# Performance work log

Measured on AMD Instinct MI355X. Metric: run time of the kernel, lower is better.

## Reference

```python
import jax, jax.numpy as jnp
import numpy as np

SPIXELS = 1000
CLASSES = 21


def setup_inputs() -> dict:
    key = jax.random.key(0)
    k1, k2, k3, k4 = jax.random.split(key, 4)
    B, H, W = 8, 512, 512
    pred = jax.random.normal(k1, (B, CLASSES, H, W), dtype=jnp.float32)
    Laplace_W_c = jax.random.normal(k2, (B, SPIXELS, SPIXELS), dtype=jnp.float32)
    Laplace_L_c = jax.random.normal(k3, (B, SPIXELS, SPIXELS), dtype=jnp.float32)
    image_spiex = jax.random.randint(k4, (B, H, W), 0, SPIXELS, dtype=jnp.int32)
    return {"pred": pred, "Laplace_W_c": Laplace_W_c, "Laplace_L_c": Laplace_L_c, "image_spiex": image_spiex}


def reference(pred, Laplace_W_c, Laplace_L_c, image_spiex):
    B, _, H, W = pred.shape
    P = H * W
    # Faithful to original: permute(0,2,3,1) then reshape to [B, class_num, H*W]
    pred_r = jnp.transpose(pred, (0, 2, 3, 1)).reshape(B, CLASSES, P)  # [B, C, P]
    seg = image_spiex.reshape(B, P)  # [B, P] superpixel ids
    # result[b, c, s] = sum_{p: seg[b,p]==s} pred_r[b, c, p]  -- the bmm(pred, one_hot_mask)
    # expressed as an efficient segment-sum instead of materializing [B, P, SPIXELS].
    seg_sum = jax.vmap(
        lambda x, ids: jax.ops.segment_sum(x, ids, num_segments=SPIXELS)
    )(jnp.transpose(pred_r, (0, 2, 1)), seg)  # [B, S, C]
    result = jnp.transpose(seg_sum, (0, 2, 1))  # [B, C, S]
    # mask.sum() = count of (b, p, s) with seg[b,p] == s, i.e. pixels with valid ids
    mask_sum = jnp.sum(((seg >= 0) & (seg < SPIXELS)).astype(pred.dtype))
    result = result / (mask_sum + 1e-16)
    # trace(R @ L @ R^T) per batch, fused
    traces = jnp.einsum('bcs,bst,bct->b', result, Laplace_L_c, result)  # [B]
    loss = (2.0 / jnp.linalg.norm(Laplace_W_c)) * traces
    return jnp.mean(loss)
```

## Files before the change

### kernel.cpp

```cpp
#include <hip/hip_runtime.h>
#include <hip/hip_bf16.h>

#define SPIX 1000
#define NCLS 21
#define PP (512*512)
#define NB_IMG 8
#define EPB (NCLS*PP)

#define FWIN 32768
#define BLKS_PER_B (EPB / FWIN)
#define DUMP 1000

#define R_OFF   0
#define TR_OFF  (NB_IMG*NCLS*SPIX)
#define NS_OFF  (TR_OFF + NB_IMG)
#define CNT_OFF (NS_OFF + 1)
#define CTR_OFF (CNT_OFF + 1)
#define WS_FLOATS (CTR_OFF + 1)

__device__ __forceinline__ void fatomic_add(float* p, float v) {
    unsafeAtomicAdd(p, v);
}

__global__ __launch_bounds__(512, 8) void scatter_kernel(const float* __restrict__ pred,
                                                         const int* __restrict__ seg,
                                                         const float* __restrict__ W,
                                                         float* __restrict__ Rout,
                                                         float* __restrict__ ns,
                                                         float* __restrict__ cnt) {
    if (blockIdx.y == NB_IMG) {
        if (blockIdx.x < 128) {
            const float4* W4 = (const float4*)W;
            const int n4 = (NB_IMG * SPIX * SPIX) / 4;
            float s = 0.f;
            for (int i = blockIdx.x * 512 + threadIdx.x; i < n4; i += 128 * 512) {
                float4 v = W4[i];
                s += v.x*v.x + v.y*v.y + v.z*v.z + v.w*v.w;
            }
            #pragma unroll
            for (int off = 32; off; off >>= 1) s += __shfl_xor(s, off);
            if ((threadIdx.x & 63) == 0) fatomic_add(ns, s);
        } else {
            const int4* s4 = (const int4*)seg;
            const int n4 = (NB_IMG * PP) / 4;
            int c = 0;
            for (int i = (blockIdx.x - 128) * 512 + threadIdx.x; i < n4; i += 40 * 512) {
                int4 v = s4[i];
                c += ((unsigned)v.x < SPIX) + ((unsigned)v.y < SPIX) + ((unsigned)v.z < SPIX) + ((unsigned)v.w < SPIX);
            }
            float f = (float)c;
            #pragma unroll
            for (int off = 32; off; off >>= 1) f += __shfl_xor(f, off);
            if ((threadIdx.x & 63) == 0) fatomic_add(cnt, f);
        }
        return;
    }
    __shared__ float         Rw[8][1024];
    __shared__ unsigned char Mk[8][1024];
    const int b    = blockIdx.y;
    const int tid  = threadIdx.x;
    const int wave = tid >> 6;
    const unsigned char lane = (unsigned char)(tid & 63);
    const unsigned f0 = (unsigned)blockIdx.x * FWIN;
    const unsigned c0 = f0 >> 18;
    const unsigned p0 = f0 & (PP - 1);

    for (int i = tid; i < 8 * 1024; i += 512) ((float*)Rw)[i] = 0.f;
    __syncthreads();

    volatile float*         vR = Rw[wave];
    volatile unsigned char* vM = Mk[wave];
    float* aR = (float*)Rw[wave];

    const float* pb   = pred + (size_t)b * EPB;
    const int*   segb = seg + (size_t)b * PP + p0;

    for (int it = 0; it < FWIN / (512 * 4); ++it) {
        const int e0 = (it * 512 + tid) * 4;
        int4 sv = *(const int4*)(segb + e0);
        int sA[4]; float vA[4];
        {
            unsigned fk = f0 + (unsigned)e0;
            unsigned sp = fk / 21u;
            unsigned ch = fk - sp * 21u;
            #pragma unroll
            for (int k = 0; k < 4; ++k) {
                vA[k] = pb[(ch << 18) + sp];
                int s = (&sv.x)[k];
                sA[k] = ((unsigned)s < SPIX) ? s : DUMP;
                ch++;
                bool c21 = (ch == 21u);
                sp += c21 ? 1u : 0u;
                ch  = c21 ? 0u : ch;
            }
        }
        #pragma unroll
        for (int i = 0; i < 3; ++i)
            #pragma unroll
            for (int j = i + 1; j < 4; ++j) {
                bool e = (sA[j] == sA[i]) && (sA[i] != DUMP);
                vA[i] += e ? vA[j] : 0.f;
                sA[j]  = e ? DUMP  : sA[j];
            }
        #pragma unroll
        for (int k = 0; k < 4; ++k) vM[sA[k]] = lane;
        unsigned char rd[4];
        #pragma unroll
        for (int k = 0; k < 4; ++k) rd[k] = vM[sA[k]];
        float od[4];
        #pragma unroll
        for (int k = 0; k < 4; ++k) od[k] = vR[sA[k]];
        bool lose1[4];
        #pragma unroll
        for (int k = 0; k < 4; ++k) {
            lose1[k] = (rd[k] != lane);
            vR[lose1[k] ? DUMP : sA[k]] = od[k] + vA[k];
        }
        asm volatile("" ::: "memory");
        #pragma unroll
        for (int k = 0; k < 4; ++k) {
            if (lose1[k]) fatomic_add(&aR[sA[k]], vA[k]);
        }
    }
    __syncthreads();

    float* Rb = Rout + (size_t)b * NCLS * SPIX + (size_t)c0 * SPIX;
    for (int i = tid; i < SPIX; i += 512) {
        float a = 0.f;
        #pragma unroll
        for (int w = 0; w < 8; ++w) a += Rw[w][i];
        fatomic_add(&Rb[i], a);
    }
}

__global__ __launch_bounds__(512) void trace_kernel(const float* __restrict__ L,
                                                    const float* __restrict__ R,
                                                    float* __restrict__ traces,
                                                    const float* __restrict__ ns,
                                                    const float* __restrict__ cnt,
                                                    unsigned* __restrict__ ctr,
                                                    float* __restrict__ out) {
    __shared__ float Rl[NCLS * SPIX];
    const int b = blockIdx.y;
    const float* Rb = R + (size_t)b * NCLS * SPIX;
    for (int i = threadIdx.x; i < NCLS * SPIX; i += 512) Rl[i] = Rb[i];
    __syncthreads();

    const int wave = threadIdx.x >> 6;
    const int lane = threadIdx.x & 63;
    const float* Lb = L + (size_t)b * SPIX * SPIX;

    const int s0 = (blockIdx.x * 8 + wave) * 4;
    bool val[4];
    const float4* Lr[4];
    #pragma unroll
    for (int r = 0; r < 4; ++r) {
        int sr = s0 + r;
        val[r] = sr < SPIX;
        Lr[r] = (const float4*)(Lb + (size_t)(val[r] ? sr : (SPIX - 1)) * SPIX);
    }

    float acc[4][NCLS];
    #pragma unroll
    for (int r = 0; r < 4; ++r)
        #pragma unroll
        for (int c = 0; c < NCLS; ++c) acc[r][c] = 0.f;

    #pragma unroll
    for (int it = 0; it < 4; ++it) {
        int idx = it * 64 + lane;
        if (idx < SPIX / 4) {
            float4 l[4];
            #pragma unroll
            for (int r = 0; r < 4; ++r)
                l[r] = val[r] ? Lr[r][idx] : make_float4(0.f, 0.f, 0.f, 0.f);
            #pragma unroll
            for (int c = 0; c < NCLS; ++c) {
                float4 rr = *(const float4*)&Rl[c * SPIX + idx * 4];
                #pragma unroll
                for (int r = 0; r < 4; ++r)
                    acc[r][c] += l[r].x * rr.x + l[r].y * rr.y + l[r].z * rr.z + l[r].w * rr.w;
            }
        }
    }

    float partial = 0.f;
    #pragma unroll
    for (int c = 0; c < NCLS; ++c)
        #pragma unroll
        for (int r = 0; r < 4; ++r)
            if (val[r]) partial += Rl[c * SPIX + s0 + r] * acc[r][c];

    #pragma unroll
    for (int off = 32; off; off >>= 1) partial += __shfl_xor(partial, off);
    if (lane == 0) fatomic_add(&traces[b], partial);

    __syncthreads();
    if (threadIdx.x == 0) {
        __threadfence();
        unsigned old = atomicAdd(ctr, 1u);
        if (old == 32u * NB_IMG - 1u) {
            __threadfence();
            float t = 0.f;
            #pragma unroll
            for (int i = 0; i < NB_IMG; ++i)
                t += __hip_atomic_load(&traces[i], __ATOMIC_RELAXED, __HIP_MEMORY_SCOPE_AGENT);
            float denom = cnt[0] + 1e-16f;
            out[0] = (2.f / sqrtf(ns[0])) * t / (denom * denom) / (float)NB_IMG;
        }
    }
}

extern "C" void kernel_launch(void* const* d_in, const int* in_sizes, int n_in,
                              void* d_out, int out_size, void* d_ws, size_t ws_size,
                              hipStream_t stream) {
    const float* pred = (const float*)d_in[0];
    const float* Wc   = (const float*)d_in[1];
    const float* Lc   = (const float*)d_in[2];
    const int*   seg  = (const int*)d_in[3];
    float* ws = (float*)d_ws;
    float* out = (float*)d_out;

    hipMemsetAsync(d_ws, 0, WS_FLOATS * sizeof(float), stream);

    scatter_kernel<<<dim3(BLKS_PER_B, NB_IMG + 1), 512, 0, stream>>>(
        pred, seg, Wc, ws + R_OFF, ws + NS_OFF, ws + CNT_OFF);

    trace_kernel<<<dim3(32, NB_IMG), 512, 0, stream>>>(
        Lc, ws + R_OFF, ws + TR_OFF, ws + NS_OFF, ws + CNT_OFF,
        (unsigned*)(ws + CTR_OFF), out);
}
```

Baseline: 158.3 us.

## Reuse per-pixel conflict analysis across all classes and reduce partials deterministically

Each block now handles a window of 4096 pixels and loops over all 21 output channels. The superpixel-ID load, the within-thread duplicate detection and the two-round LDS conflict election run once per window instead of once per class window, and the resulting masks are reused for every class. Per-class block results go either to a partial buffer reduced by a new reduce_kernel, which avoids global atomics, or to atomics when the workspace is too small. The trade-offs are an extra kernel launch and partial-buffer traffic, lower occupancy (launch bounds drop to 4), and fewer blocks for the W-norm and count side tasks.

```diff
diff --git a/kernel.cpp b/kernel.cpp
--- a/kernel.cpp
+++ b/kernel.cpp
@@ -7,8 +7,9 @@
 #define NB_IMG 8
 #define EPB (NCLS*PP)
 
-#define FWIN 32768
-#define BLKS_PER_B (EPB / FWIN)
+#define WIN 4096
+#define WPB (PP/WIN)
+#define NBLK (WPB*NB_IMG)
 #define DUMP 1000
 
 #define R_OFF   0
@@ -17,23 +18,27 @@
 #define CNT_OFF (NS_OFF + 1)
 #define CTR_OFF (CNT_OFF + 1)
 #define WS_FLOATS (CTR_OFF + 1)
+#define RP_OFF  ((WS_FLOATS + 3) & ~3)
+#define RP_FLOATS ((size_t)NBLK * NCLS * SPIX)
 
 __device__ __forceinline__ void fatomic_add(float* p, float v) {
     unsafeAtomicAdd(p, v);
 }
 
-__global__ __launch_bounds__(512, 8) void scatter_kernel(const float* __restrict__ pred,
+__global__ __launch_bounds__(512, 4) void scatter_kernel(const float* __restrict__ pred,
                                                          const int* __restrict__ seg,
                                                          const float* __restrict__ W,
                                                          float* __restrict__ Rout,
+                                                         float* __restrict__ Rp,
+                                                         int use_part,
                                                          float* __restrict__ ns,
                                                          float* __restrict__ cnt) {
     if (blockIdx.y == NB_IMG) {
-        if (blockIdx.x < 128) {
+        if (blockIdx.x < 48) {
             const float4* W4 = (const float4*)W;
             const int n4 = (NB_IMG * SPIX * SPIX) / 4;
             float s = 0.f;
-            for (int i = blockIdx.x * 512 + threadIdx.x; i < n4; i += 128 * 512) {
+            for (int i = blockIdx.x * 512 + threadIdx.x; i < n4; i += 48 * 512) {
                 float4 v = W4[i];
                 s += v.x*v.x + v.y*v.y + v.z*v.z + v.w*v.w;
             }
@@ -44,7 +49,7 @@
             const int4* s4 = (const int4*)seg;
             const int n4 = (NB_IMG * PP) / 4;
             int c = 0;
-            for (int i = (blockIdx.x - 128) * 512 + threadIdx.x; i < n4; i += 40 * 512) {
+            for (int i = (blockIdx.x - 48) * 512 + threadIdx.x; i < n4; i += 16 * 512) {
                 int4 v = s4[i];
                 c += ((unsigned)v.x < SPIX) + ((unsigned)v.y < SPIX) + ((unsigned)v.z < SPIX) + ((unsigned)v.w < SPIX);
             }
@@ -58,15 +63,13 @@
     __shared__ float         Rw[8][1024];
     __shared__ unsigned char Mk[8][1024];
     const int b    = blockIdx.y;
+    const int wb   = blockIdx.x;
     const int tid  = threadIdx.x;
     const int wave = tid >> 6;
     const unsigned char lane = (unsigned char)(tid & 63);
-    const unsigned f0 = (unsigned)blockIdx.x * FWIN;
-    const unsigned c0 = f0 >> 18;
-    const unsigned p0 = f0 & (PP - 1);
+    const unsigned p0 = (unsigned)wb * WIN;
 
     for (int i = tid; i < 8 * 1024; i += 512) ((float*)Rw)[i] = 0.f;
-    __syncthreads();
 
     volatile float*         vR = Rw[wave];
     volatile unsigned char* vM = Mk[wave];
@@ -75,61 +78,125 @@
     const float* pb   = pred + (size_t)b * EPB;
     const int*   segb = seg + (size_t)b * PP + p0;
 
-    for (int it = 0; it < FWIN / (512 * 4); ++it) {
-        const int e0 = (it * 512 + tid) * 4;
-        int4 sv = *(const int4*)(segb + e0);
-        int sA[4]; float vA[4];
-        {
-            unsigned fk = f0 + (unsigned)e0;
+    unsigned sA[8];
+    unsigned m_w1 = 0, m_w2 = 0, m_fb = 0, firsts = 0;
+    #pragma unroll
+    for (int st = 0; st < 2; ++st) {
+        int4 sv = *(const int4*)(segb + st * 2048 + tid * 4);
+        unsigned s0 = ((unsigned)sv.x < SPIX) ? (unsigned)sv.x : DUMP;
+        unsigned s1 = ((unsigned)sv.y < SPIX) ? (unsigned)sv.y : DUMP;
+        unsigned s2 = ((unsigned)sv.z < SPIX) ? (unsigned)sv.z : DUMP;
+        unsigned s3 = ((unsigned)sv.w < SPIX) ? (unsigned)sv.w : DUMP;
+        unsigned f1 = (s1 == s0) ? 0u : 1u;
+        unsigned f2 = (s2 == s0) ? 0u : ((s2 == s1) ? 1u : 2u);
+        unsigned f3 = (s3 == s0) ? 0u : ((s3 == s1) ? 1u : ((s3 == s2) ? 2u : 3u));
+        firsts |= (f1 | (f2 << 2) | (f3 << 4)) << (st * 8);
+        if (f1 != 1u) s1 = DUMP;
+        if (f2 != 2u) s2 = DUMP;
+        if (f3 != 3u) s3 = DUMP;
+        sA[st*4+0] = s0; sA[st*4+1] = s1; sA[st*4+2] = s2; sA[st*4+3] = s3;
+        #pragma unroll
+        for (int k = 0; k < 4; ++k) vM[sA[st*4+k]] = lane;
+        unsigned char rd[4];
+        #pragma unroll
+        for (int k = 0; k < 4; ++k) rd[k] = vM[sA[st*4+k]];
+        unsigned a2[4];
+        #pragma unroll
+        for (int k = 0; k < 4; ++k) a2[k] = (rd[k] == lane) ? 1008u : sA[st*4+k];
+        #pragma unroll
+        for (int k = 0; k < 4; ++k) vM[a2[k]] = lane;
+        unsigned char rd2[4];
+        #pragma unroll
+        for (int k = 0; k < 4; ++k) rd2[k] = vM[a2[k]];
+        #pragma unroll
+        for (int k = 0; k < 4; ++k) {
+            bool w1 = (rd[k] == lane);
+            bool w2 = (rd2[k] == lane) && !w1;
+            bool fb = !w1 && !w2 && (sA[st*4+k] != DUMP);
+            m_w1 |= (w1 ? 1u : 0u) << (st*4+k);
+            m_w2 |= (w2 ? 1u : 0u) << (st*4+k);
+            m_fb |= (fb ? 1u : 0u) << (st*4+k);
+        }
+    }
+    __syncthreads();
+
+    const bool mtid = (tid < 250);
+    #pragma unroll 1
+    for (int c = 0; c < NCLS; ++c) {
+        #pragma unroll
+        for (int st = 0; st < 2; ++st) {
+            unsigned fk = (unsigned)c * PP + p0 + (unsigned)(st * 2048 + tid * 4);
             unsigned sp = fk / 21u;
             unsigned ch = fk - sp * 21u;
+            float vA[4];
             #pragma unroll
             for (int k = 0; k < 4; ++k) {
                 vA[k] = pb[(ch << 18) + sp];
-                int s = (&sv.x)[k];
-                sA[k] = ((unsigned)s < SPIX) ? s : DUMP;
                 ch++;
-                bool c21 = (ch == 21u);
-                sp += c21 ? 1u : 0u;
-                ch  = c21 ? 0u : ch;
-            }
-        }
-        #pragma unroll
-        for (int i = 0; i < 3; ++i)
-            #pragma unroll
-            for (int j = i + 1; j < 4; ++j) {
-                bool e = (sA[j] == sA[i]) && (sA[i] != DUMP);
-                vA[i] += e ? vA[j] : 0.f;
-                sA[j]  = e ? DUMP  : sA[j];
-            }
-        #pragma unroll
-        for (int k = 0; k < 4; ++k) vM[sA[k]] = lane;
-        unsigned char rd[4];
-        #pragma unroll
-        for (int k = 0; k < 4; ++k) rd[k] = vM[sA[k]];
-        float od[4];
-        #pragma unroll
-        for (int k = 0; k < 4; ++k) od[k] = vR[sA[k]];
-        bool lose1[4];
-        #pragma unroll
-        for (int k = 0; k < 4; ++k) {
-            lose1[k] = (rd[k] != lane);
-            vR[lose1[k] ? DUMP : sA[k]] = od[k] + vA[k];
-        }
-        asm volatile("" ::: "memory");
-        #pragma unroll
-        for (int k = 0; k < 4; ++k) {
-            if (lose1[k]) fatomic_add(&aR[sA[k]], vA[k]);
-        }
-    }
-    __syncthreads();
-
-    float* Rb = Rout + (size_t)b * NCLS * SPIX + (size_t)c0 * SPIX;
-    for (int i = tid; i < SPIX; i += 512) {
-        float a = 0.f;
-        #pragma unroll
-        for (int w = 0; w < 8; ++w) a += Rw[w][i];
-        fatomic_add(&Rb[i], a);
+                bool cc = (ch == 21u);
+                sp += cc ? 1u : 0u;
+                ch  = cc ? 0u : ch;
+            }
+            unsigned fst = firsts >> (st * 8);
+            unsigned f1 = fst & 3u, f2 = (fst >> 2) & 3u, f3 = (fst >> 4) & 3u;
+            vA[0] += (f1 == 0u) ? vA[1] : 0.f;
+            vA[0] += (f2 == 0u) ? vA[2] : 0.f;
+            vA[1] += (f2 == 1u) ? vA[2] : 0.f;
+            vA[0] += (f3 == 0u) ? vA[3] : 0.f;
+            vA[1] += (f3 == 1u) ? vA[3] : 0.f;
+            vA[2] += (f3 == 2u) ? vA[3] : 0.f;
+            unsigned mw1 = m_w1 >> (st*4), mw2 = m_w2 >> (st*4), mfb = m_fb >> (st*4);
+            float od[4];
+            #pragma unroll
+            for (int k = 0; k < 4; ++k) od[k] = vR[sA[st*4+k]];
+            #pragma unroll
+            for (int k = 0; k < 4; ++k)
+                vR[((mw1 >> k) & 1u) ? sA[st*4+k] : (1016u + k)] = od[k] + vA[k];
+            float od2[4];
+            #pragma unroll
+            for (int k = 0; k < 4; ++k) od2[k] = vR[sA[st*4+k]];
+            #pragma unroll
+            for (int k = 0; k < 4; ++k)
+                vR[((mw2 >> k) & 1u) ? sA[st*4+k] : (1016u + k)] = od2[k] + vA[k];
+            asm volatile("" ::: "memory");
+            #pragma unroll
+            for (int k = 0; k < 4; ++k)
+                if ((mfb >> k) & 1u) fatomic_add(&aR[sA[st*4+k]], vA[k]);
+        }
+        __syncthreads();
+        if (mtid) {
+            float4 a = make_float4(0.f, 0.f, 0.f, 0.f);
+            #pragma unroll
+            for (int w = 0; w < 8; ++w) {
+                float4 t = ((const float4*)Rw[w])[tid];
+                a.x += t.x; a.y += t.y; a.z += t.z; a.w += t.w;
+                ((float4*)Rw[w])[tid] = make_float4(0.f, 0.f, 0.f, 0.f);
+            }
+            if (use_part) {
+                ((float4*)(Rp + ((size_t)(b * WPB + wb) * NCLS + c) * SPIX))[tid] = a;
+            } else {
+                float* dst = Rout + ((size_t)b * NCLS + c) * SPIX + tid * 4;
+                fatomic_add(dst + 0, a.x);
+                fatomic_add(dst + 1, a.y);
+                fatomic_add(dst + 2, a.z);
+                fatomic_add(dst + 3, a.w);
+            }
+        }
+        __syncthreads();
+    }
+}
+
+__global__ __launch_bounds__(256) void reduce_kernel(const float* __restrict__ Rp,
+                                                     float* __restrict__ Rout) {
+    const int c = blockIdx.x, b = blockIdx.y, tid = threadIdx.x;
+    if (tid < 250) {
+        float4 a = make_float4(0.f, 0.f, 0.f, 0.f);
+        #pragma unroll 4
+        for (int w = 0; w < WPB; ++w) {
+            float4 t = ((const float4*)(Rp + ((size_t)(b * WPB + w) * NCLS + c) * SPIX))[tid];
+            a.x += t.x; a.y += t.y; a.z += t.z; a.w += t.w;
+        }
+        ((float4*)(Rout + ((size_t)b * NCLS + c) * SPIX))[tid] = a;
     }
 }
 
@@ -221,10 +288,16 @@
     float* ws = (float*)d_ws;
     float* out = (float*)d_out;
 
+    const size_t need = ((size_t)RP_OFF + RP_FLOATS) * sizeof(float);
+    const int use_part = (ws_size >= need) ? 1 : 0;
+
     hipMemsetAsync(d_ws, 0, WS_FLOATS * sizeof(float), stream);
 
-    scatter_kernel<<<dim3(BLKS_PER_B, NB_IMG + 1), 512, 0, stream>>>(
-        pred, seg, Wc, ws + R_OFF, ws + NS_OFF, ws + CNT_OFF);
+    scatter_kernel<<<dim3(WPB, NB_IMG + 1), 512, 0, stream>>>(
+        pred, seg, Wc, ws + R_OFF, ws + RP_OFF, use_part, ws + NS_OFF, ws + CNT_OFF);
+
+    if (use_part)
+        reduce_kernel<<<dim3(NCLS, NB_IMG), 256, 0, stream>>>(ws + RP_OFF, ws + R_OFF);
 
     trace_kernel<<<dim3(32, NB_IMG), 512, 0, stream>>>(
         Lc, ws + R_OFF, ws + TR_OFF, ws + NS_OFF, ws + CNT_OFF,
```

New measurement: 201.6 us. +27.4%, slower.
